# Performance work log

Measured on AMD Instinct MI355X. Metric: run time of the kernel, lower is better.

## Reference

```python
import jax, jax.numpy as jnp
import numpy as np

N_AGENTS = 32
UNIT_DIM = 64
HIDDEN = 128
BATCH = 1024
STATE_DIM = 128


def setup_inputs() -> dict:
    key = jax.random.key(0)
    ks = jax.random.split(key, 8)
    s = 0.05
    return {
        "state": jax.random.normal(ks[0], (BATCH, STATE_DIM), dtype=jnp.float32),
        "unit_states": jax.random.normal(ks[1], (N_AGENTS, BATCH, UNIT_DIM), dtype=jnp.float32),
        # edge_predictor params, stored [in, out] so y = x @ W + b (matches torch Linear math)
        "W1": jax.random.normal(ks[2], (2 * UNIT_DIM, HIDDEN), dtype=jnp.float32) * s,
        "b1": jnp.zeros((HIDDEN,), dtype=jnp.float32),
        "W2": jax.random.normal(ks[3], (HIDDEN, HIDDEN), dtype=jnp.float32) * s,
        "b2": jnp.zeros((HIDDEN,), dtype=jnp.float32),
        "W3": jax.random.normal(ks[4], (HIDDEN, 1), dtype=jnp.float32) * s,
        "b3": jnp.zeros((1,), dtype=jnp.float32),
    }


def reference(state, unit_states, W1, b1, W2, b2, W3, b3):
    # unit_states: [n_agents, B, d] -> [B, n_agents, d]  (permute(1,0,2))
    us = jnp.transpose(unit_states, (1, 0, 2))
    d = us.shape[-1]
    # Pairwise concat [us_i, us_j] through the first Linear is equivalent to
    # splitting W1 into its i-half and j-half and broadcast-adding (same math,
    # avoids materializing the [B,n,n,2d] concat tensor). Dropout rate is 0.0
    # (eval-mode identity).
    hi = us @ W1[:d]   # [B, n, H]
    hj = us @ W1[d:]   # [B, n, H]
    h = jax.nn.relu(hi[:, :, None, :] + hj[:, None, :, :] + b1)  # [B, n, n, H]
    h = jax.nn.relu(h @ W2 + b2)                                  # [B, n, n, H]
    logits = (h @ W3 + b3)[..., 0]                                # [B, n, n]
    adj = jax.nn.sigmoid(logits)
    # graph_add_self_loop = True
    adj = adj + jnp.eye(adj.shape[-1], dtype=adj.dtype)[None]
    return adj
```

## Files before the change

kernel.cpp:

```cpp
#include <hip/hip_runtime.h>
#include <hip/hip_bf16.h>

#define BATCH 1024
#define NA 32
#define UD 64
#define HID 128

typedef _Float16 f16x8 __attribute__((ext_vector_type(8)));
typedef float f32x4 __attribute__((ext_vector_type(4)));

__global__ void prep_weights(const float* __restrict__ W1,
                             const float* __restrict__ W2,
                             _Float16* __restrict__ ws)
{
    int tid  = blockIdx.x * blockDim.x + threadIdx.x;
    int unit = tid >> 6;
    int lane = tid & 63;
    int l15  = lane & 15;
    int lq   = lane >> 4;
    f16x8 v;
    if (unit < 32) {
        int ks = unit >> 3, nt = unit & 7;
        int col = nt * 16 + l15;
        int k0  = ks * 32 + lq * 8;
        #pragma unroll
        for (int e = 0; e < 8; ++e)
            v[e] = (_Float16)W2[(k0 + e) * HID + col];
    } else {
        int u = unit - 32;
        int h = u >> 4, ks = (u >> 3) & 1, nt = u & 7;
        int col = nt * 16 + l15;
        int k0  = ks * 32 + lq * 8;
        #pragma unroll
        for (int e = 0; e < 8; ++e)
            v[e] = (_Float16)W1[(h * UD + k0 + e) * HID + col];
    }
    *(f16x8*)&ws[(size_t)(unit * 64 + lane) * 8] = v;
}

template <bool FROM_WS>
__global__ __launch_bounds__(256, 2)
void graph_learner_kernel(const float* __restrict__ us_g,
                          const float* __restrict__ W1,
                          const float* __restrict__ b1,
                          const float* __restrict__ W2,
                          const float* __restrict__ b2,
                          const float* __restrict__ W3,
                          const float* __restrict__ b3,
                          const _Float16* __restrict__ ws,
                          float* __restrict__ out)
{
    __shared__ _Float16 us_f16[NA * UD]  __attribute__((aligned(16)));
    __shared__ _Float16 hi_lds[NA * HID] __attribute__((aligned(16)));
    __shared__ _Float16 hj_lds[NA * HID] __attribute__((aligned(16)));

    const int b    = blockIdx.x;
    const int t    = threadIdx.x;
    const int w    = t >> 6;
    const int lane = t & 63;
    const int l15  = lane & 15;
    const int lq   = lane >> 4;

    {
        int i  = t >> 3;
        int c  = t & 7;
        const float* src = us_g + ((size_t)i * BATCH + (size_t)b) * UD + c * 8;
        float4 va = *(const float4*)src;
        float4 vb = *(const float4*)(src + 4);
        f16x8 v8;
        v8[0] = (_Float16)va.x; v8[1] = (_Float16)va.y;
        v8[2] = (_Float16)va.z; v8[3] = (_Float16)va.w;
        v8[4] = (_Float16)vb.x; v8[5] = (_Float16)vb.y;
        v8[6] = (_Float16)vb.z; v8[7] = (_Float16)vb.w;
        *(f16x8*)&us_f16[i * UD + ((c ^ (i & 7)) << 3)] = v8;
    }

    f32x4 b2q[8], w3q[8];
    #pragma unroll
    for (int nt = 0; nt < 8; ++nt) {
        b2q[nt] = *(const f32x4*)&b2[nt * 16 + lq * 4];
        w3q[nt] = *(const f32x4*)&W3[nt * 16 + lq * 4];
    }
    const float b3s = b3[0];

    const int Mt = w >> 1;
    const int nh = w & 1;

    f16x8 w1f[4][2][2];
    float b1v[4];
    #pragma unroll
    for (int n = 0; n < 4; ++n) {
        int nt = nh * 4 + n;
        b1v[n] = b1[nt * 16 + l15];
        if (FROM_WS) {
            #pragma unroll
            for (int h = 0; h < 2; ++h)
                #pragma unroll
                for (int ks = 0; ks < 2; ++ks) {
                    int u = 32 + h * 16 + ks * 8 + nt;
                    w1f[n][h][ks] = *(const f16x8*)&ws[(size_t)(u * 64 + lane) * 8];
                }
        } else {
            int col = nt * 16 + l15;
            #pragma unroll
            for (int h = 0; h < 2; ++h)
                #pragma unroll
                for (int ks = 0; ks < 2; ++ks)
                    #pragma unroll
                    for (int e = 0; e < 8; ++e)
                        w1f[n][h][ks][e] = (_Float16)W1[(h * UD + ks * 32 + lq * 8 + e) * HID + col];
        }
    }

    __syncthreads();

    {
        f16x8 af[2];
        #pragma unroll
        for (int ks = 0; ks < 2; ++ks) {
            int row = Mt * 16 + l15;
            int c   = ks * 4 + lq;
            af[ks] = *(const f16x8*)&us_f16[row * UD + ((c ^ (row & 7)) << 3)];
        }
        #pragma unroll
        for (int n = 0; n < 4; ++n) {
            int nt = nh * 4 + n;
            f32x4 ahi = {b1v[n], b1v[n], b1v[n], b1v[n]};
            f32x4 ahj = {0.f, 0.f, 0.f, 0.f};
            #pragma unroll
            for (int ks = 0; ks < 2; ++ks) {
                ahi = __builtin_amdgcn_mfma_f32_16x16x32_f16(af[ks], w1f[n][0][ks], ahi, 0, 0, 0);
                ahj = __builtin_amdgcn_mfma_f32_16x16x32_f16(af[ks], w1f[n][1][ks], ahj, 0, 0, 0);
            }
            #pragma unroll
            for (int r = 0; r < 4; ++r) {
                int row = Mt * 16 + lq * 4 + r;
                int col = nt * 16 + l15;
                int idx = row * HID + ((((col >> 3) ^ (row & 15)) << 3) + (col & 7));
                hi_lds[idx] = (_Float16)ahi[r];
                hj_lds[idx] = (_Float16)ahj[r];
            }
        }
    }

    f16x8 w2f[32];
    if (FROM_WS) {
        #pragma unroll
        for (int q = 0; q < 32; ++q)
            w2f[q] = *(const f16x8*)&ws[(size_t)(q * 64 + lane) * 8];
    } else {
        #pragma unroll
        for (int ks = 0; ks < 4; ++ks)
            #pragma unroll
            for (int nt = 0; nt < 8; ++nt) {
                int col = nt * 16 + l15;
                int k0  = ks * 32 + lq * 8;
                #pragma unroll
                for (int e = 0; e < 8; ++e)
                    w2f[ks * 8 + nt][e] = (_Float16)W2[(k0 + e) * HID + col];
            }
    }

    __syncthreads();

    #pragma unroll
    for (int q = 0; q < 32; q += 4)
        asm volatile("" : "+v"(w2f[q]), "+v"(w2f[q + 1]), "+v"(w2f[q + 2]), "+v"(w2f[q + 3]));

    #pragma unroll 1
    for (int tt = 0; tt < 16; ++tt) {
        const int mt = w + tt * 4;
        const int i  = mt >> 1;
        const int j  = ((mt & 1) << 4) + l15;
        const _Float16* hir = &hi_lds[i * HID];
        const _Float16* hjr = &hj_lds[j * HID];
        const int isz = i & 15, jsz = j & 15;

        f32x4 acc[8];
        #pragma unroll
        for (int nt = 0; nt < 8; ++nt) acc[nt] = b2q[nt];

        #pragma unroll
        for (int ks = 0; ks < 4; ++ks) {
            int c0 = ks * 4 + lq;
            f16x8 hi8 = *(const f16x8*)&hir[(c0 ^ isz) << 3];
            f16x8 hj8 = *(const f16x8*)&hjr[(c0 ^ jsz) << 3];
            f16x8 s   = hi8 + hj8;
            f16x8 z   = {};
            f16x8 xb  = __builtin_elementwise_max(s, z);
            #pragma unroll
            for (int nt = 0; nt < 8; ++nt)
                acc[nt] = __builtin_amdgcn_mfma_f32_16x16x32_f16(w2f[ks * 8 + nt], xb, acc[nt], 0, 0, 0);
        }

        float p = 0.f;
        #pragma unroll
        for (int nt = 0; nt < 8; ++nt) {
            p += fmaxf(acc[nt][0], 0.f) * w3q[nt][0];
            p += fmaxf(acc[nt][1], 0.f) * w3q[nt][1];
            p += fmaxf(acc[nt][2], 0.f) * w3q[nt][2];
            p += fmaxf(acc[nt][3], 0.f) * w3q[nt][3];
        }
        p += __shfl_xor(p, 16);
        p += __shfl_xor(p, 32);

        float x  = p + b3s;
        float sg = 1.f / (1.f + __expf(-x));
        int   pi = mt * 16 + l15;
        sg += ((pi >> 5) == (pi & 31)) ? 1.f : 0.f;
        if (lane < 16)
            out[(size_t)b * (NA * NA) + pi] = sg;
    }
}

extern "C" void kernel_launch(void* const* d_in, const int* in_sizes, int n_in,
                              void* d_out, int out_size, void* d_ws, size_t ws_size,
                              hipStream_t stream) {
    const float* us = (const float*)d_in[1];
    const float* W1 = (const float*)d_in[2];
    const float* b1 = (const float*)d_in[3];
    const float* W2 = (const float*)d_in[4];
    const float* b2 = (const float*)d_in[5];
    const float* W3 = (const float*)d_in[6];
    const float* b3 = (const float*)d_in[7];
    float* out = (float*)d_out;
    _Float16* ws = (_Float16*)d_ws;

    const bool use_ws = (ws_size >= 64u * 64u * 8u * sizeof(_Float16));
    if (use_ws) {
        prep_weights<<<dim3(16), dim3(256), 0, stream>>>(W1, W2, ws);
        graph_learner_kernel<true><<<dim3(BATCH), dim3(256), 0, stream>>>(
            us, W1, b1, W2, b2, W3, b3, ws, out);
    } else {
        graph_learner_kernel<false><<<dim3(BATCH), dim3(256), 0, stream>>>(
            us, W1, b1, W2, b2, W3, b3, ws, out);
    }
}
```

Baseline: 116.1 us.

## Switch layer-2 GEMM to 32x32x16 MFMA with W2 staged in LDS

Replaces the 16x16x32 MFMA tiling of the second Linear layer with 32x32x16 MFMAs, so each wave processes one full i-row (32 j's) per iteration and hj rows are loaded once. W2 fragments move from 32 persistent VGPR vectors into shared memory and are re-read every iteration, which frees registers. W3 is also moved to LDS and the prep layout is rewritten to match. It also drops the fallback path that ran without a workspace. In exchange it adds about 32KB of LDS per block and extra LDS reads of W2 inside the main loop.

```diff
diff --git a/kernel.cpp b/kernel.cpp
--- a/kernel.cpp
+++ b/kernel.cpp
@@ -8,6 +8,7 @@
 
 typedef _Float16 f16x8 __attribute__((ext_vector_type(8)));
 typedef float f32x4 __attribute__((ext_vector_type(4)));
+typedef float f32x16 __attribute__((ext_vector_type(16)));
 
 __global__ void prep_weights(const float* __restrict__ W1,
                              const float* __restrict__ W2,
@@ -16,34 +17,29 @@
     int tid  = blockIdx.x * blockDim.x + threadIdx.x;
     int unit = tid >> 6;
     int lane = tid & 63;
-    int l15  = lane & 15;
-    int lq   = lane >> 4;
     f16x8 v;
     if (unit < 32) {
-        int ks = unit >> 3, nt = unit & 7;
-        int col = nt * 16 + l15;
-        int k0  = ks * 32 + lq * 8;
+        int m  = unit >> 3, ks = unit & 7;
+        int h  = m * 32 + (lane & 31);
+        int k0 = ks * 16 + (lane >> 5) * 8;
         #pragma unroll
         for (int e = 0; e < 8; ++e)
-            v[e] = (_Float16)W2[(k0 + e) * HID + col];
+            v[e] = (_Float16)W2[(k0 + e) * HID + h];
     } else {
         int u = unit - 32;
-        int h = u >> 4, ks = (u >> 3) & 1, nt = u & 7;
-        int col = nt * 16 + l15;
-        int k0  = ks * 32 + lq * 8;
+        int hh = u >> 4, ks = (u >> 3) & 1, nt = u & 7;
+        int col = nt * 16 + (lane & 15);
+        int k0  = ks * 32 + (lane >> 4) * 8;
         #pragma unroll
         for (int e = 0; e < 8; ++e)
-            v[e] = (_Float16)W1[(h * UD + k0 + e) * HID + col];
+            v[e] = (_Float16)W1[(hh * UD + k0 + e) * HID + col];
     }
     *(f16x8*)&ws[(size_t)(unit * 64 + lane) * 8] = v;
 }
 
-template <bool FROM_WS>
 __global__ __launch_bounds__(256, 2)
 void graph_learner_kernel(const float* __restrict__ us_g,
-                          const float* __restrict__ W1,
                           const float* __restrict__ b1,
-                          const float* __restrict__ W2,
                           const float* __restrict__ b2,
                           const float* __restrict__ W3,
                           const float* __restrict__ b3,
@@ -53,6 +49,8 @@
     __shared__ _Float16 us_f16[NA * UD]  __attribute__((aligned(16)));
     __shared__ _Float16 hi_lds[NA * HID] __attribute__((aligned(16)));
     __shared__ _Float16 hj_lds[NA * HID] __attribute__((aligned(16)));
+    __shared__ _Float16 w2_lds[32 * 64 * 8] __attribute__((aligned(16)));
+    __shared__ float    w3_lds[HID] __attribute__((aligned(16)));
 
     const int b    = blockIdx.x;
     const int t    = threadIdx.x;
@@ -60,6 +58,8 @@
     const int lane = t & 63;
     const int l15  = lane & 15;
     const int lq   = lane >> 4;
+    const int l31  = lane & 31;
+    const int hi2  = lane >> 5;
 
     {
         int i  = t >> 3;
@@ -75,41 +75,45 @@
         *(f16x8*)&us_f16[i * UD + ((c ^ (i & 7)) << 3)] = v8;
     }
 
-    f32x4 b2q[8], w3q[8];
+    {
+        const f16x8* src = (const f16x8*)ws;
+        f16x8*       dst = (f16x8*)w2_lds;
+        #pragma unroll
+        for (int q = 0; q < 8; ++q) {
+            int s = q * 256 + t;
+            dst[s] = src[s];
+        }
+    }
+    if (t < 32)
+        *(f32x4*)&w3_lds[t * 4] = *(const f32x4*)&W3[t * 4];
+
+    f32x16 b2q[4];
     #pragma unroll
-    for (int nt = 0; nt < 8; ++nt) {
-        b2q[nt] = *(const f32x4*)&b2[nt * 16 + lq * 4];
-        w3q[nt] = *(const f32x4*)&W3[nt * 16 + lq * 4];
-    }
+    for (int m = 0; m < 4; ++m)
+        #pragma unroll
+        for (int g = 0; g < 4; ++g) {
+            f32x4 v = *(const f32x4*)&b2[m * 32 + g * 8 + hi2 * 4];
+            #pragma unroll
+            for (int s = 0; s < 4; ++s)
+                b2q[m][g * 4 + s] = v[s];
+        }
     const float b3s = b3[0];
 
     const int Mt = w >> 1;
     const int nh = w & 1;
-
     f16x8 w1f[4][2][2];
     float b1v[4];
     #pragma unroll
     for (int n = 0; n < 4; ++n) {
         int nt = nh * 4 + n;
         b1v[n] = b1[nt * 16 + l15];
-        if (FROM_WS) {
-            #pragma unroll
-            for (int h = 0; h < 2; ++h)
-                #pragma unroll
-                for (int ks = 0; ks < 2; ++ks) {
-                    int u = 32 + h * 16 + ks * 8 + nt;
-                    w1f[n][h][ks] = *(const f16x8*)&ws[(size_t)(u * 64 + lane) * 8];
-                }
-        } else {
-            int col = nt * 16 + l15;
-            #pragma unroll
-            for (int h = 0; h < 2; ++h)
-                #pragma unroll
-                for (int ks = 0; ks < 2; ++ks)
-                    #pragma unroll
-                    for (int e = 0; e < 8; ++e)
-                        w1f[n][h][ks][e] = (_Float16)W1[(h * UD + ks * 32 + lq * 8 + e) * HID + col];
-        }
+        #pragma unroll
+        for (int h = 0; h < 2; ++h)
+            #pragma unroll
+            for (int ks = 0; ks < 2; ++ks) {
+                int u = 32 + h * 16 + ks * 8 + nt;
+                w1f[n][h][ks] = *(const f16x8*)&ws[(size_t)(u * 64 + lane) * 8];
+            }
     }
 
     __syncthreads();
@@ -143,73 +147,54 @@
         }
     }
 
-    f16x8 w2f[32];
-    if (FROM_WS) {
-        #pragma unroll
-        for (int q = 0; q < 32; ++q)
-            w2f[q] = *(const f16x8*)&ws[(size_t)(q * 64 + lane) * 8];
-    } else {
-        #pragma unroll
-        for (int ks = 0; ks < 4; ++ks)
-            #pragma unroll
-            for (int nt = 0; nt < 8; ++nt) {
-                int col = nt * 16 + l15;
-                int k0  = ks * 32 + lq * 8;
-                #pragma unroll
-                for (int e = 0; e < 8; ++e)
-                    w2f[ks * 8 + nt][e] = (_Float16)W2[(k0 + e) * HID + col];
-            }
-    }
-
     __syncthreads();
 
-    #pragma unroll
-    for (int q = 0; q < 32; q += 4)
-        asm volatile("" : "+v"(w2f[q]), "+v"(w2f[q + 1]), "+v"(w2f[q + 2]), "+v"(w2f[q + 3]));
+    const _Float16* hjr = &hj_lds[l31 * HID];
+    const int jsz = l31 & 15;
 
     #pragma unroll 1
-    for (int tt = 0; tt < 16; ++tt) {
-        const int mt = w + tt * 4;
-        const int i  = mt >> 1;
-        const int j  = ((mt & 1) << 4) + l15;
+    for (int tt = 0; tt < 8; ++tt) {
+        asm volatile("" ::: "memory");
+        const int i   = w + tt * 4;
+        const int isz = i & 15;
         const _Float16* hir = &hi_lds[i * HID];
-        const _Float16* hjr = &hj_lds[j * HID];
-        const int isz = i & 15, jsz = j & 15;
-
-        f32x4 acc[8];
-        #pragma unroll
-        for (int nt = 0; nt < 8; ++nt) acc[nt] = b2q[nt];
-
-        #pragma unroll
-        for (int ks = 0; ks < 4; ++ks) {
-            int c0 = ks * 4 + lq;
-            f16x8 hi8 = *(const f16x8*)&hir[(c0 ^ isz) << 3];
-            f16x8 hj8 = *(const f16x8*)&hjr[(c0 ^ jsz) << 3];
-            f16x8 s   = hi8 + hj8;
-            f16x8 z   = {};
-            f16x8 xb  = __builtin_elementwise_max(s, z);
-            #pragma unroll
-            for (int nt = 0; nt < 8; ++nt)
-                acc[nt] = __builtin_amdgcn_mfma_f32_16x16x32_f16(w2f[ks * 8 + nt], xb, acc[nt], 0, 0, 0);
-        }
-
-        float p = 0.f;
-        #pragma unroll
-        for (int nt = 0; nt < 8; ++nt) {
-            p += fmaxf(acc[nt][0], 0.f) * w3q[nt][0];
-            p += fmaxf(acc[nt][1], 0.f) * w3q[nt][1];
-            p += fmaxf(acc[nt][2], 0.f) * w3q[nt][2];
-            p += fmaxf(acc[nt][3], 0.f) * w3q[nt][3];
-        }
-        p += __shfl_xor(p, 16);
+
+        f32x16 acc[4];
+        #pragma unroll
+        for (int ks = 0; ks < 8; ++ks) {
+            int c = ks * 2 + hi2;
+            f16x8 h8 = *(const f16x8*)&hir[(c ^ isz) << 3];
+            f16x8 g8 = *(const f16x8*)&hjr[(c ^ jsz) << 3];
+            f16x8 s  = h8 + g8;
+            f16x8 z  = {};
+            f16x8 xb = __builtin_elementwise_max(s, z);
+            #pragma unroll
+            for (int m = 0; m < 4; ++m) {
+                f16x8 wf = *(const f16x8*)&w2_lds[(size_t)((m * 8 + ks) * 64 + lane) * 8];
+                acc[m] = __builtin_amdgcn_mfma_f32_32x32x16_f16(
+                    wf, xb, (ks == 0) ? b2q[m] : acc[m], 0, 0, 0);
+            }
+        }
+
+        float pa = 0.f, pb = 0.f;
+        #pragma unroll
+        for (int m = 0; m < 4; ++m)
+            #pragma unroll
+            for (int g = 0; g < 4; ++g) {
+                f32x4 w3v = *(const f32x4*)&w3_lds[m * 32 + g * 8 + hi2 * 4];
+                pa += fmaxf(acc[m][g * 4 + 0], 0.f) * w3v[0];
+                pb += fmaxf(acc[m][g * 4 + 1], 0.f) * w3v[1];
+                pa += fmaxf(acc[m][g * 4 + 2], 0.f) * w3v[2];
+                pb += fmaxf(acc[m][g * 4 + 3], 0.f) * w3v[3];
+            }
+        float p = pa + pb;
         p += __shfl_xor(p, 32);
 
         float x  = p + b3s;
         float sg = 1.f / (1.f + __expf(-x));
-        int   pi = mt * 16 + l15;
-        sg += ((pi >> 5) == (pi & 31)) ? 1.f : 0.f;
-        if (lane < 16)
-            out[(size_t)b * (NA * NA) + pi] = sg;
+        if (l31 == i) sg += 1.f;
+        if (lane < 32)
+            out[(size_t)b * (NA * NA) + i * 32 + l31] = sg;
     }
 }
 
@@ -226,13 +211,7 @@
     float* out = (float*)d_out;
     _Float16* ws = (_Float16*)d_ws;
 
-    const bool use_ws = (ws_size >= 64u * 64u * 8u * sizeof(_Float16));
-    if (use_ws) {
-        prep_weights<<<dim3(16), dim3(256), 0, stream>>>(W1, W2, ws);
-        graph_learner_kernel<true><<<dim3(BATCH), dim3(256), 0, stream>>>(
-            us, W1, b1, W2, b2, W3, b3, ws, out);
-    } else {
-        graph_learner_kernel<false><<<dim3(BATCH), dim3(256), 0, stream>>>(
-            us, W1, b1, W2, b2, W3, b3, ws, out);
-    }
+    prep_weights<<<dim3(16), dim3(256), 0, stream>>>(W1, W2, ws);
+    graph_learner_kernel<<<dim3(BATCH), dim3(256), 0, stream>>>(
+        us, b1, b2, W3, b3, ws, out);
 }
```

New measurement: 119.3 us. 1.03x slower.
